# Kernel tuning notes

Measured on AMD Instinct MI355X. Metric: run time of the kernel, lower is better.

Reference implementation:

```python
import jax, jax.numpy as jnp
import numpy as np

NA, NKPT, NC = 3, 17, 1
NO_DET = NC + 5              # 6
NO = NO_DET + 3 * NKPT       # 57
ANCHORS = np.array([[19,27,44,40,38,94],[96,68,86,152,180,137],[140,301,303,264,238,542]], dtype=np.float32).reshape(3, 3, 2)
STRIDES = np.array([8.0, 16.0, 32.0], dtype=np.float32)
CH = (256, 512, 1024)
HW = (80, 40, 20)
B = 16


def setup_inputs():
    key = jax.random.key(0)
    ks = jax.random.split(key, 18)
    d = {}
    ki = 0
    for i, (c, hw) in enumerate(zip(CH, HW)):
        d[f"f{i}"] = jax.random.normal(ks[ki], (B, c, hw, hw), jnp.float32); ki += 1
        d[f"ia{i}"] = jax.random.normal(ks[ki], (1, c, 1, 1), jnp.float32) * 0.02; ki += 1
        d[f"w{i}"] = jax.random.normal(ks[ki], (NA * NO_DET, c), jnp.float32) * (1.0 / np.sqrt(c)); ki += 1
        d[f"b{i}"] = jnp.zeros((NA * NO_DET,), jnp.float32)
        d[f"im{i}"] = 1.0 + jax.random.normal(ks[ki], (1, NA * NO_DET, 1, 1), jnp.float32) * 0.02; ki += 1
        d[f"wk{i}"] = jax.random.normal(ks[ki], (NA * 3 * NKPT, c), jnp.float32) * (1.0 / np.sqrt(c)); ki += 1
        d[f"bk{i}"] = jnp.zeros((NA * 3 * NKPT,), jnp.float32)
    return d


def _decode(feat, ia, w, b, im, wk, bk, anchors_l, stride):
    # ImplicitA -> 1x1 conv -> ImplicitM (det branch); plain 1x1 conv (kpt branch)
    det = jnp.einsum('bchw,oc->bohw', feat + ia, w) + b[None, :, None, None]
    det = det * im
    kpt = jnp.einsum('bchw,oc->bohw', feat, wk) + bk[None, :, None, None]
    x = jnp.concatenate([det, kpt], axis=1)          # (B, na*no, H, W)
    Bb, _, H, W = x.shape
    x = x.reshape(Bb, NA, NO, H, W).transpose(0, 1, 3, 4, 2)  # (B, na, H, W, no)
    yv, xv = jnp.meshgrid(jnp.arange(H), jnp.arange(W), indexing='ij')
    grid = jnp.stack([xv, yv], -1).astype(x.dtype)[None, None]  # (1,1,H,W,2)
    xd = jax.nn.sigmoid(x[..., :NO_DET])
    xy = (xd[..., 0:2] * 2.0 - 0.5 + grid) * stride
    wh = (xd[..., 2:4] * 2.0) ** 2 * anchors_l.reshape(1, NA, 1, 1, 2)
    kp = x[..., NO_DET:]                              # (B, na, H, W, 51)
    kx = (kp[..., 0::3] * 2.0 - 0.5 + grid[..., 0:1]) * stride
    ky = (kp[..., 1::3] * 2.0 - 0.5 + grid[..., 1:2]) * stride
    kc = jax.nn.sigmoid(kp[..., 2::3])
    kdec = jnp.stack([kx, ky, kc], -1).reshape(Bb, NA, H, W, 3 * NKPT)
    y = jnp.concatenate([xy, wh, xd[..., 4:], kdec], -1)  # (B, na, H, W, 57)
    return y.reshape(Bb, -1, NO)


def reference(f0, ia0, w0, b0, im0, wk0, bk0,
              f1, ia1, w1, b1, im1, wk1, bk1,
              f2, ia2, w2, b2, im2, wk2, bk2):
    anchors = jnp.asarray(ANCHORS)
    z0 = _decode(f0, ia0, w0, b0, im0, wk0, bk0, anchors[0], STRIDES[0])
    z1 = _decode(f1, ia1, w1, b1, im1, wk1, bk1, anchors[1], STRIDES[1])
    z2 = _decode(f2, ia2, w2, b2, im2, wk2, bk2, anchors[2], STRIDES[2])
    return jnp.concatenate([z0, z1, z2], axis=1)      # (B, 25200, 57)
```

## Files before the change

### kernel.cpp

```cpp
#include <hip/hip_runtime.h>
#include <hip/hip_bf16.h>

typedef __attribute__((ext_vector_type(8))) short short8;
typedef __attribute__((ext_vector_type(4))) float floatx4;

__device__ __forceinline__ float sigm(float x) { return 1.0f / (1.0f + __expf(-x)); }

__device__ __forceinline__ unsigned short f2bf(float v) {
  union { __hip_bfloat16 h; unsigned short u; } cv;
  cv.h = __float2bfloat16(v);
  return cv.u;
}

__global__ void prep_kernel(const float* __restrict__ w, const float* __restrict__ b,
                            const float* __restrict__ im, const float* __restrict__ ia,
                            const float* __restrict__ wk, const float* __restrict__ bk,
                            unsigned short* __restrict__ Wp, float* __restrict__ bias, int C) {
  const int n = blockIdx.x;
  const int t = threadIdx.x;
  unsigned short* wrow = Wp + (size_t)n * C;
  if (n >= 171) {
    for (int k = t; k < C; k += 64) wrow[k] = 0;
    if (t == 0) bias[n] = 0.0f;
    return;
  }
  if (n < 18) {
    const float* src = w + (size_t)n * C;
    const float sc = im[n];
    float dot = 0.0f;
    for (int k = t; k < C; k += 64) {
      float v = src[k];
      dot += v * ia[k];
      wrow[k] = f2bf(v * sc);
    }
#pragma unroll
    for (int off = 32; off > 0; off >>= 1) dot += __shfl_down(dot, off);
    if (t == 0) bias[n] = sc * (b[n] + dot);
  } else {
    const float* src = wk + (size_t)(n - 18) * C;
    for (int k = t; k < C; k += 64) wrow[k] = f2bf(src[k]);
    if (t == 0) bias[n] = bk[n - 18];
  }
}

#define SMEM_BYTES 46080

template <int SC, int C, int HW, int W>
__device__ __forceinline__ void gemm_decode(const float* __restrict__ feat,
                                            const unsigned short* __restrict__ Wp,
                                            const float* __restrict__ bias,
                                            float* __restrict__ out, int tile, char* smem) {
  constexpr float STRD = (SC == 0) ? 8.0f : (SC == 1) ? 16.0f : 32.0f;
  constexpr int ZOFF = (SC == 0) ? 0 : (SC == 1) ? 19200 : 24000;
  constexpr int AST = 72;
  constexpr int BST = 72;
  constexpr int EST = 180;

  const int t = threadIdx.x;
  const int lane = t & 63;
  const int wv = t >> 6;
  const int l15 = lane & 15;
  const int quad = lane >> 4;

  unsigned short* Alds = (unsigned short*)smem;
  unsigned short* Blds = (unsigned short*)(smem + 9216);
  float* Elds = (float*)smem;

  const int m0 = tile * 64;
  const int mA = m0 + lane;
  const int bA = mA / HW;
  const int pA = mA - bA * HW;
  const float* fbase = feat + ((size_t)bA * C) * HW + pA + (size_t)(wv * 16) * HW;

  floatx4 acc[11];
#pragma unroll
  for (int j = 0; j < 11; ++j) acc[j] = (floatx4){0.f, 0.f, 0.f, 0.f};

  const unsigned short* aRd = Alds + (wv * 16 + l15) * AST + quad * 8;
  const unsigned short* bRd = Blds + l15 * BST + quad * 8;

  const int k8 = (t & 7) * 8;
  const int nr = t >> 3;

  for (int k0 = 0; k0 < C; k0 += 64) {
    __syncthreads();
    {
      const float* g = fbase + (size_t)k0 * HW;
      float v[16];
#pragma unroll
      for (int kk = 0; kk < 16; ++kk) v[kk] = g[(size_t)kk * HW];
      short8 s0, s1;
#pragma unroll
      for (int kk = 0; kk < 8; ++kk) {
        s0[kk] = (short)f2bf(v[kk]);
        s1[kk] = (short)f2bf(v[kk + 8]);
      }
      *(short8*)(Alds + lane * AST + wv * 16) = s0;
      *(short8*)(Alds + lane * AST + wv * 16 + 8) = s1;
    }
#pragma unroll
    for (int pp = 0; pp < 6; ++pp) {
      int n = pp * 32 + nr;
      if (n < 176) {
        short8 wv8 = *(const short8*)(Wp + (size_t)n * C + k0 + k8);
        *(short8*)(Blds + n * BST + k8) = wv8;
      }
    }
    __syncthreads();
#pragma unroll
    for (int h = 0; h < 2; ++h) {
      short8 af = *(const short8*)(aRd + h * 32);
#pragma unroll
      for (int j = 0; j < 11; ++j) {
        short8 bf = *(const short8*)(bRd + j * 16 * BST + h * 32);
        acc[j] = __builtin_amdgcn_mfma_f32_16x16x32_bf16(af, bf, acc[j], 0, 0, 0);
      }
    }
  }

  __syncthreads();
#pragma unroll
  for (int j = 0; j < 11; ++j) {
    float bj = bias[j * 16 + l15];
#pragma unroll
    for (int r = 0; r < 4; ++r) {
      int row = wv * 16 + quad * 4 + r;
      Elds[row * EST + j * 16 + l15] = acc[j][r] + bj;
    }
  }
  __syncthreads();
  if (t < 192) {
    const int rr = t & 63;
    const int a = t >> 6;
    const int m = m0 + rr;
    const int bb = m / HW;
    const int p = m - bb * HW;
    const float fx = (float)(p % W);
    const float fy = (float)(p / W);
    float aw, ah;
    if constexpr (SC == 0) {
      aw = (a == 0) ? 19.f : (a == 1) ? 44.f : 38.f;
      ah = (a == 0) ? 27.f : (a == 1) ? 40.f : 94.f;
    } else if constexpr (SC == 1) {
      aw = (a == 0) ? 96.f : (a == 1) ? 86.f : 180.f;
      ah = (a == 0) ? 68.f : (a == 1) ? 152.f : 137.f;
    } else {
      aw = (a == 0) ? 140.f : (a == 1) ? 303.f : 238.f;
      ah = (a == 0) ? 301.f : (a == 1) ? 264.f : 542.f;
    }
    float* L = Elds + rr * EST + a * 57;
    float r0 = L[0], r1 = L[1], r2 = L[2], r3 = L[3], r4 = L[4], r5 = L[5];
    L[0] = (sigm(r0) * 2.f - 0.5f + fx) * STRD;
    L[1] = (sigm(r1) * 2.f - 0.5f + fy) * STRD;
    float tw = sigm(r2) * 2.f;
    L[2] = tw * tw * aw;
    float th = sigm(r3) * 2.f;
    L[3] = th * th * ah;
    L[4] = sigm(r4);
    L[5] = sigm(r5);
#pragma unroll
    for (int kp = 0; kp < 17; ++kp) {
      float kx = L[6 + 3 * kp], ky = L[7 + 3 * kp], kc = L[8 + 3 * kp];
      L[6 + 3 * kp] = (kx * 2.f - 0.5f + fx) * STRD;
      L[7 + 3 * kp] = (ky * 2.f - 0.5f + fy) * STRD;
      L[8 + 3 * kp] = sigm(kc);
    }
  }
  __syncthreads();
  for (int i = t; i < 192 * 57; i += 256) {
    int row = i / 57;
    int jj = i - row * 57;
    int a = row >> 6, rr = row & 63;
    int m = m0 + rr;
    int bb = m / HW;
    int p = m - bb * HW;
    size_t orow = (size_t)bb * 25200 + (size_t)(ZOFF + a * HW + p);
    out[orow * 57 + jj] = Elds[rr * EST + a * 57 + jj];
  }
}

__global__ __launch_bounds__(256, 3) void main_kernel(
    const float* __restrict__ f0, const float* __restrict__ f1, const float* __restrict__ f2,
    const unsigned short* __restrict__ Wp0, const unsigned short* __restrict__ Wp1,
    const unsigned short* __restrict__ Wp2, const float* __restrict__ b0,
    const float* __restrict__ b1, const float* __restrict__ b2, float* __restrict__ out) {
  __shared__ __align__(16) char smem[SMEM_BYTES];
  const int bid = blockIdx.x;
  if (bid < 100)
    gemm_decode<2, 1024, 400, 20>(f2, Wp2, b2, out, bid, smem);
  else if (bid < 500)
    gemm_decode<1, 512, 1600, 40>(f1, Wp1, b1, out, bid - 100, smem);
  else
    gemm_decode<0, 256, 6400, 80>(f0, Wp0, b0, out, bid - 500, smem);
}

extern "C" void kernel_launch(void* const* d_in, const int* in_sizes, int n_in, void* d_out,
                              int out_size, void* d_ws, size_t ws_size, hipStream_t stream) {
  const float *f[3], *ia[3], *w[3], *b[3], *im[3], *wk[3], *bk[3];
  for (int s = 0; s < 3; ++s) {
    f[s] = (const float*)d_in[7 * s + 0];
    ia[s] = (const float*)d_in[7 * s + 1];
    w[s] = (const float*)d_in[7 * s + 2];
    b[s] = (const float*)d_in[7 * s + 3];
    im[s] = (const float*)d_in[7 * s + 4];
    wk[s] = (const float*)d_in[7 * s + 5];
    bk[s] = (const float*)d_in[7 * s + 6];
  }
  char* ws = (char*)d_ws;
  unsigned short* Wp0 = (unsigned short*)(ws + 0);
  unsigned short* Wp1 = (unsigned short*)(ws + 90112);
  unsigned short* Wp2 = (unsigned short*)(ws + 270336);
  float* bias0 = (float*)(ws + 630784);
  float* bias1 = (float*)(ws + 631488);
  float* bias2 = (float*)(ws + 632192);

  const int Cs[3] = {256, 512, 1024};
  unsigned short* Wps[3] = {Wp0, Wp1, Wp2};
  float* biases[3] = {bias0, bias1, bias2};
  for (int s = 0; s < 3; ++s)
    prep_kernel<<<176, 64, 0, stream>>>(w[s], b[s], im[s], ia[s], wk[s], bk[s], Wps[s],
                                        biases[s], Cs[s]);
  main_kernel<<<2100, 256, 0, stream>>>(f[0], f[1], f[2], Wp0, Wp1, Wp2, bias0, bias1, bias2,
                                        (float*)d_out);
}
```

Before: 318.9 us.

## Double-buffer per-wave A tiles, read weights from global, enlarge M tile

Each wave now stages its own 32-row A slice in a double-buffered LDS region without block-wide barriers. The next k-step's fp32 loads are issued while the current MFMAs run. B fragments are read straight from global/L2 instead of being staged through LDS, and each block covers 128 rows, so half as many blocks are launched. The epilogue runs in four 32-row chunks so it fits the smaller LDS footprint. The three prep launches are merged into one. Costs are higher register pressure (launch bounds drop to 2 blocks per CU) and uncached repeated global reads of the weights.

```diff
diff --git a/kernel.cpp b/kernel.cpp
--- a/kernel.cpp
+++ b/kernel.cpp
@@ -12,38 +12,44 @@
   return cv.u;
 }
 
-__global__ void prep_kernel(const float* __restrict__ w, const float* __restrict__ b,
-                            const float* __restrict__ im, const float* __restrict__ ia,
-                            const float* __restrict__ wk, const float* __restrict__ bk,
-                            unsigned short* __restrict__ Wp, float* __restrict__ bias, int C) {
+struct PrepArgs {
+  const float *w, *b, *im, *ia, *wk, *bk;
+  unsigned short* Wp;
+  float* bias;
+  int C;
+};
+
+__global__ void prep_kernel(PrepArgs A0, PrepArgs A1, PrepArgs A2) {
+  PrepArgs A = (blockIdx.y == 0) ? A0 : (blockIdx.y == 1) ? A1 : A2;
   const int n = blockIdx.x;
   const int t = threadIdx.x;
-  unsigned short* wrow = Wp + (size_t)n * C;
+  const int C = A.C;
+  unsigned short* wrow = A.Wp + (size_t)n * C;
   if (n >= 171) {
     for (int k = t; k < C; k += 64) wrow[k] = 0;
-    if (t == 0) bias[n] = 0.0f;
+    if (t == 0) A.bias[n] = 0.0f;
     return;
   }
   if (n < 18) {
-    const float* src = w + (size_t)n * C;
-    const float sc = im[n];
+    const float* src = A.w + (size_t)n * C;
+    const float sc = A.im[n];
     float dot = 0.0f;
     for (int k = t; k < C; k += 64) {
       float v = src[k];
-      dot += v * ia[k];
+      dot += v * A.ia[k];
       wrow[k] = f2bf(v * sc);
     }
 #pragma unroll
     for (int off = 32; off > 0; off >>= 1) dot += __shfl_down(dot, off);
-    if (t == 0) bias[n] = sc * (b[n] + dot);
+    if (t == 0) A.bias[n] = sc * (A.b[n] + dot);
   } else {
-    const float* src = wk + (size_t)(n - 18) * C;
+    const float* src = A.wk + (size_t)(n - 18) * C;
     for (int k = t; k < C; k += 64) wrow[k] = f2bf(src[k]);
-    if (t == 0) bias[n] = bk[n - 18];
-  }
-}
-
-#define SMEM_BYTES 46080
+    if (t == 0) A.bias[n] = A.bk[n - 18];
+  }
+}
+
+#define LDS_BYTES 36864
 
 template <int SC, int C, int HW, int W>
 __device__ __forceinline__ void gemm_decode(const float* __restrict__ feat,
@@ -52,9 +58,7 @@
                                             float* __restrict__ out, int tile, char* smem) {
   constexpr float STRD = (SC == 0) ? 8.0f : (SC == 1) ? 16.0f : 32.0f;
   constexpr int ZOFF = (SC == 0) ? 0 : (SC == 1) ? 19200 : 24000;
-  constexpr int AST = 72;
-  constexpr int BST = 72;
-  constexpr int EST = 180;
+  constexpr int I = C / 64;
 
   const int t = threadIdx.x;
   const int lane = t & 63;
@@ -63,135 +67,162 @@
   const int quad = lane >> 4;
 
   unsigned short* Alds = (unsigned short*)smem;
-  unsigned short* Blds = (unsigned short*)(smem + 9216);
   float* Elds = (float*)smem;
 
-  const int m0 = tile * 64;
-  const int mA = m0 + lane;
-  const int bA = mA / HW;
-  const int pA = mA - bA * HW;
-  const float* fbase = feat + ((size_t)bA * C) * HW + pA + (size_t)(wv * 16) * HW;
-
-  floatx4 acc[11];
-#pragma unroll
-  for (int j = 0; j < 11; ++j) acc[j] = (floatx4){0.f, 0.f, 0.f, 0.f};
-
-  const unsigned short* aRd = Alds + (wv * 16 + l15) * AST + quad * 8;
-  const unsigned short* bRd = Blds + l15 * BST + quad * 8;
-
-  const int k8 = (t & 7) * 8;
-  const int nr = t >> 3;
-
-  for (int k0 = 0; k0 < C; k0 += 64) {
+  const int r = lane & 31;
+  const int kh = lane >> 5;
+  const int mG = tile * 128 + wv * 32 + r;
+  const int bA = mG / HW;
+  const int pA = mG - bA * HW;
+  const float* gL = feat + ((size_t)bA * C + kh * 32) * (size_t)HW + pA;
+
+  floatx4 acc[2][11];
+#pragma unroll
+  for (int mi = 0; mi < 2; ++mi)
+#pragma unroll
+    for (int nj = 0; nj < 11; ++nj) acc[mi][nj] = (floatx4){0.f, 0.f, 0.f, 0.f};
+
+  const unsigned short* bP = Wp + (size_t)l15 * C + quad * 8;
+  unsigned short* wD = Alds + wv * 4608 + r * 72 + kh * 32;
+  const unsigned short* aB = Alds + wv * 4608 + l15 * 72 + quad * 8;
+
+  float v[32];
+  auto loadA = [&](int it) {
+    const float* g = gL + (size_t)it * 64 * HW;
+#pragma unroll
+    for (int kk = 0; kk < 32; ++kk) v[kk] = g[(size_t)kk * HW];
+  };
+  auto writeA = [&](int pb) {
+    unsigned short* d = wD + pb * 2304;
+#pragma unroll
+    for (int c8 = 0; c8 < 4; ++c8) {
+      short8 s;
+#pragma unroll
+      for (int j = 0; j < 8; ++j) s[j] = (short)f2bf(v[c8 * 8 + j]);
+      *(short8*)(d + c8 * 8) = s;
+    }
+  };
+  auto mfmaStep = [&](int it) {
+    const int pb = it & 1;
+    const unsigned short* a = aB + pb * 2304;
+    short8 af[2][2];
+#pragma unroll
+    for (int mi = 0; mi < 2; ++mi)
+#pragma unroll
+      for (int h = 0; h < 2; ++h) af[mi][h] = *(const short8*)(a + mi * 1152 + h * 32);
+    const unsigned short* bI = bP + it * 64;
+#pragma unroll
+    for (int nj = 0; nj < 11; ++nj) {
+      short8 b0 = *(const short8*)(bI + (size_t)nj * 16 * C);
+      short8 b1 = *(const short8*)(bI + (size_t)nj * 16 * C + 32);
+      acc[0][nj] = __builtin_amdgcn_mfma_f32_16x16x32_bf16(af[0][0], b0, acc[0][nj], 0, 0, 0);
+      acc[1][nj] = __builtin_amdgcn_mfma_f32_16x16x32_bf16(af[1][0], b0, acc[1][nj], 0, 0, 0);
+      acc[0][nj] = __builtin_amdgcn_mfma_f32_16x16x32_bf16(af[0][1], b1, acc[0][nj], 0, 0, 0);
+      acc[1][nj] = __builtin_amdgcn_mfma_f32_16x16x32_bf16(af[1][1], b1, acc[1][nj], 0, 0, 0);
+    }
+  };
+
+  loadA(0);
+#pragma unroll
+  for (int it = 0; it < I - 1; ++it) {
+    writeA(it & 1);
+    loadA(it + 1);
+    mfmaStep(it);
+  }
+  writeA((I - 1) & 1);
+  mfmaStep(I - 1);
+
+  float bj[11];
+#pragma unroll
+  for (int nj = 0; nj < 11; ++nj) bj[nj] = bias[nj * 16 + l15];
+
+#pragma unroll
+  for (int c = 0; c < 4; ++c) {
     __syncthreads();
-    {
-      const float* g = fbase + (size_t)k0 * HW;
-      float v[16];
-#pragma unroll
-      for (int kk = 0; kk < 16; ++kk) v[kk] = g[(size_t)kk * HW];
-      short8 s0, s1;
-#pragma unroll
-      for (int kk = 0; kk < 8; ++kk) {
-        s0[kk] = (short)f2bf(v[kk]);
-        s1[kk] = (short)f2bf(v[kk + 8]);
+    if (wv == c) {
+#pragma unroll
+      for (int nj = 0; nj < 11; ++nj)
+#pragma unroll
+        for (int mi = 0; mi < 2; ++mi)
+#pragma unroll
+          for (int rr = 0; rr < 4; ++rr)
+            Elds[(mi * 16 + quad * 4 + rr) * 180 + nj * 16 + l15] = acc[mi][nj][rr] + bj[nj];
+    }
+    __syncthreads();
+    if (t < 192) {
+      const int task = t >> 1, half = t & 1;
+      const int row = task & 31, a = task >> 5;
+      const int m = tile * 128 + c * 32 + row;
+      const int bb = m / HW;
+      const int p = m - bb * HW;
+      const float fx = (float)(p % W);
+      const float fy = (float)(p / W);
+      float* L = Elds + row * 180 + a * 57;
+      if (half == 0) {
+        float aw, ah;
+        if constexpr (SC == 0) {
+          aw = (a == 0) ? 19.f : (a == 1) ? 44.f : 38.f;
+          ah = (a == 0) ? 27.f : (a == 1) ? 40.f : 94.f;
+        } else if constexpr (SC == 1) {
+          aw = (a == 0) ? 96.f : (a == 1) ? 86.f : 180.f;
+          ah = (a == 0) ? 68.f : (a == 1) ? 152.f : 137.f;
+        } else {
+          aw = (a == 0) ? 140.f : (a == 1) ? 303.f : 238.f;
+          ah = (a == 0) ? 301.f : (a == 1) ? 264.f : 542.f;
+        }
+        float r0 = L[0], r1 = L[1], r2 = L[2], r3 = L[3], r4 = L[4], r5 = L[5];
+        L[0] = (sigm(r0) * 2.f - 0.5f + fx) * STRD;
+        L[1] = (sigm(r1) * 2.f - 0.5f + fy) * STRD;
+        float tw = sigm(r2) * 2.f;
+        L[2] = tw * tw * aw;
+        float th = sigm(r3) * 2.f;
+        L[3] = th * th * ah;
+        L[4] = sigm(r4);
+        L[5] = sigm(r5);
+#pragma unroll
+        for (int kp = 0; kp < 8; ++kp) {
+          float kx = L[6 + 3 * kp], ky = L[7 + 3 * kp], kc = L[8 + 3 * kp];
+          L[6 + 3 * kp] = (kx * 2.f - 0.5f + fx) * STRD;
+          L[7 + 3 * kp] = (ky * 2.f - 0.5f + fy) * STRD;
+          L[8 + 3 * kp] = sigm(kc);
+        }
+      } else {
+#pragma unroll
+        for (int kp = 8; kp < 17; ++kp) {
+          float kx = L[6 + 3 * kp], ky = L[7 + 3 * kp], kc = L[8 + 3 * kp];
+          L[6 + 3 * kp] = (kx * 2.f - 0.5f + fx) * STRD;
+          L[7 + 3 * kp] = (ky * 2.f - 0.5f + fy) * STRD;
+          L[8 + 3 * kp] = sigm(kc);
+        }
       }
-      *(short8*)(Alds + lane * AST + wv * 16) = s0;
-      *(short8*)(Alds + lane * AST + wv * 16 + 8) = s1;
-    }
-#pragma unroll
-    for (int pp = 0; pp < 6; ++pp) {
-      int n = pp * 32 + nr;
-      if (n < 176) {
-        short8 wv8 = *(const short8*)(Wp + (size_t)n * C + k0 + k8);
-        *(short8*)(Blds + n * BST + k8) = wv8;
-      }
     }
     __syncthreads();
-#pragma unroll
-    for (int h = 0; h < 2; ++h) {
-      short8 af = *(const short8*)(aRd + h * 32);
-#pragma unroll
-      for (int j = 0; j < 11; ++j) {
-        short8 bf = *(const short8*)(bRd + j * 16 * BST + h * 32);
-        acc[j] = __builtin_amdgcn_mfma_f32_16x16x32_bf16(af, bf, acc[j], 0, 0, 0);
-      }
-    }
-  }
-
-  __syncthreads();
-#pragma unroll
-  for (int j = 0; j < 11; ++j) {
-    float bj = bias[j * 16 + l15];
-#pragma unroll
-    for (int r = 0; r < 4; ++r) {
-      int row = wv * 16 + quad * 4 + r;
-      Elds[row * EST + j * 16 + l15] = acc[j][r] + bj;
-    }
-  }
-  __syncthreads();
-  if (t < 192) {
-    const int rr = t & 63;
-    const int a = t >> 6;
-    const int m = m0 + rr;
-    const int bb = m / HW;
-    const int p = m - bb * HW;
-    const float fx = (float)(p % W);
-    const float fy = (float)(p / W);
-    float aw, ah;
-    if constexpr (SC == 0) {
-      aw = (a == 0) ? 19.f : (a == 1) ? 44.f : 38.f;
-      ah = (a == 0) ? 27.f : (a == 1) ? 40.f : 94.f;
-    } else if constexpr (SC == 1) {
-      aw = (a == 0) ? 96.f : (a == 1) ? 86.f : 180.f;
-      ah = (a == 0) ? 68.f : (a == 1) ? 152.f : 137.f;
-    } else {
-      aw = (a == 0) ? 140.f : (a == 1) ? 303.f : 238.f;
-      ah = (a == 0) ? 301.f : (a == 1) ? 264.f : 542.f;
-    }
-    float* L = Elds + rr * EST + a * 57;
-    float r0 = L[0], r1 = L[1], r2 = L[2], r3 = L[3], r4 = L[4], r5 = L[5];
-    L[0] = (sigm(r0) * 2.f - 0.5f + fx) * STRD;
-    L[1] = (sigm(r1) * 2.f - 0.5f + fy) * STRD;
-    float tw = sigm(r2) * 2.f;
-    L[2] = tw * tw * aw;
-    float th = sigm(r3) * 2.f;
-    L[3] = th * th * ah;
-    L[4] = sigm(r4);
-    L[5] = sigm(r5);
-#pragma unroll
-    for (int kp = 0; kp < 17; ++kp) {
-      float kx = L[6 + 3 * kp], ky = L[7 + 3 * kp], kc = L[8 + 3 * kp];
-      L[6 + 3 * kp] = (kx * 2.f - 0.5f + fx) * STRD;
-      L[7 + 3 * kp] = (ky * 2.f - 0.5f + fy) * STRD;
-      L[8 + 3 * kp] = sigm(kc);
-    }
-  }
-  __syncthreads();
-  for (int i = t; i < 192 * 57; i += 256) {
-    int row = i / 57;
-    int jj = i - row * 57;
-    int a = row >> 6, rr = row & 63;
-    int m = m0 + rr;
-    int bb = m / HW;
-    int p = m - bb * HW;
-    size_t orow = (size_t)bb * 25200 + (size_t)(ZOFF + a * HW + p);
-    out[orow * 57 + jj] = Elds[rr * EST + a * 57 + jj];
-  }
-}
-
-__global__ __launch_bounds__(256, 3) void main_kernel(
+    for (int i = t; i < 96 * 57; i += 256) {
+      int sr = i / 57;
+      int j = i - sr * 57;
+      int a = sr >> 5, row = sr & 31;
+      int m = tile * 128 + c * 32 + row;
+      int bb = m / HW;
+      int p = m - bb * HW;
+      out[((size_t)bb * 25200 + (size_t)(ZOFF + a * HW + p)) * 57 + j] =
+          Elds[row * 180 + a * 57 + j];
+    }
+  }
+}
+
+__global__ __launch_bounds__(256, 2) void main_kernel(
     const float* __restrict__ f0, const float* __restrict__ f1, const float* __restrict__ f2,
     const unsigned short* __restrict__ Wp0, const unsigned short* __restrict__ Wp1,
     const unsigned short* __restrict__ Wp2, const float* __restrict__ b0,
     const float* __restrict__ b1, const float* __restrict__ b2, float* __restrict__ out) {
-  __shared__ __align__(16) char smem[SMEM_BYTES];
+  __shared__ __align__(16) char smem[LDS_BYTES];
   const int bid = blockIdx.x;
-  if (bid < 100)
+  if (bid < 50)
     gemm_decode<2, 1024, 400, 20>(f2, Wp2, b2, out, bid, smem);
-  else if (bid < 500)
-    gemm_decode<1, 512, 1600, 40>(f1, Wp1, b1, out, bid - 100, smem);
+  else if (bid < 250)
+    gemm_decode<1, 512, 1600, 40>(f1, Wp1, b1, out, bid - 50, smem);
   else
-    gemm_decode<0, 256, 6400, 80>(f0, Wp0, b0, out, bid - 500, smem);
+    gemm_decode<0, 256, 6400, 80>(f0, Wp0, b0, out, bid - 250, smem);
 }
 
 extern "C" void kernel_launch(void* const* d_in, const int* in_sizes, int n_in, void* d_out,
@@ -214,12 +245,11 @@
   float* bias1 = (float*)(ws + 631488);
   float* bias2 = (float*)(ws + 632192);
 
-  const int Cs[3] = {256, 512, 1024};
-  unsigned short* Wps[3] = {Wp0, Wp1, Wp2};
-  float* biases[3] = {bias0, bias1, bias2};
-  for (int s = 0; s < 3; ++s)
-    prep_kernel<<<176, 64, 0, stream>>>(w[s], b[s], im[s], ia[s], wk[s], bk[s], Wps[s],
-                                        biases[s], Cs[s]);
-  main_kernel<<<2100, 256, 0, stream>>>(f[0], f[1], f[2], Wp0, Wp1, Wp2, bias0, bias1, bias2,
+  PrepArgs A0 = {w[0], b[0], im[0], ia[0], wk[0], bk[0], Wp0, bias0, 256};
+  PrepArgs A1 = {w[1], b[1], im[1], ia[1], wk[1], bk[1], Wp1, bias1, 512};
+  PrepArgs A2 = {w[2], b[2], im[2], ia[2], wk[2], bk[2], Wp2, bias2, 1024};
+  prep_kernel<<<dim3(176, 3), 64, 0, stream>>>(A0, A1, A2);
+
+  main_kernel<<<1050, 256, 0, stream>>>(f[0], f[1], f[2], Wp0, Wp1, Wp2, bias0, bias1, bias2,
                                         (float*)d_out);
 }
```

Result: slower. 341.7 us (+7.2%).
